# Kernel optimization log

Measured on AMD Instinct MI355X. Metric: run time of the kernel, lower is better.

Reference implementation:

```python
import jax, jax.numpy as jnp
import numpy as np
import math

S, B, H, NH = 2048, 2, 2048, 16
HD = H // NH
COEFF = 1.0  # layer_number = 1
NORM = math.sqrt(HD) * COEFF
MASK_VAL = -10000.0


def setup_inputs() -> dict:
    key = jax.random.key(0)
    ks = jax.random.split(key, 4)
    hidden_states = jax.random.normal(ks[0], (S, B, H), dtype=jnp.float32)
    # causal mask: True = masked (Megatron convention)
    attention_mask = jnp.triu(jnp.ones((S, S), dtype=bool), k=1)[None, None]
    w_qkv = jax.random.normal(ks[1], (H, 3 * H), dtype=jnp.float32) * (1.0 / math.sqrt(H))
    b_qkv = jnp.zeros((3 * H,), dtype=jnp.float32)
    w_dense = jax.random.normal(ks[2], (H, H), dtype=jnp.float32) * (1.0 / math.sqrt(H))
    b_dense = jnp.zeros((H,), dtype=jnp.float32)
    return {"hidden_states": hidden_states, "attention_mask": attention_mask,
            "w_qkv": w_qkv, "b_qkv": b_qkv, "w_dense": w_dense, "b_dense": b_dense}


def reference(hidden_states, attention_mask, w_qkv, b_qkv, w_dense, b_dense):
    s, b, h = hidden_states.shape
    # QKV projection: [s, b, 3h] -> [s, b, nh, 3*hd] -> split
    mixed = hidden_states @ w_qkv + b_qkv
    mixed = mixed.reshape(s, b, NH, 3 * HD)
    q, k, v = jnp.split(mixed, 3, axis=-1)  # each [s, b, nh, hd]
    # raw scores scaled by 1/(sqrt(hd)*coeff)  -> [b, nh, s_q, s_k]
    scores = jnp.einsum('sbnd,tbnd->bnst', q, k) / NORM
    # fused scale-mask-softmax in fp32 with scale=coeff (net 1/sqrt(hd))
    scores32 = scores.astype(jnp.float32) * COEFF
    scores32 = jnp.where(attention_mask, MASK_VAL, scores32)
    probs = jax.nn.softmax(scores32, axis=-1).astype(hidden_states.dtype)
    # dropout p=0.0 -> identity
    context = jnp.einsum('bnst,tbnd->sbnd', probs, v).reshape(s, b, h)
    # row-parallel dense with skip_bias_add: bias returned separately
    output = context @ w_dense
    return output, b_dense
```

## Files before the change

### kernel.cpp

```cpp
#include <hip/hip_runtime.h>
#include <hip/hip_bf16.h>

constexpr int S   = 2048;
constexpr int B   = 2;
constexpr int H   = 2048;
constexpr int NH  = 16;
constexpr int HD  = 128;
constexpr int K3H = 3 * H;
constexpr float SCALE2 = 0.08838834764831845f * 1.4426950408889634f;
constexpr float MSHIFT = 12.0f;

typedef __attribute__((ext_vector_type(8))) short short8;
typedef __attribute__((ext_vector_type(4))) float f32x4;

__device__ __forceinline__ ushort f2b(float f) {
  uint u = __float_as_uint(f);
  return (ushort)((u + 0x7fffu + ((u >> 16) & 1u)) >> 16);
}

__device__ __forceinline__ f32x4 mfma16(short8 a, short8 b, f32x4 c) {
  return __builtin_amdgcn_mfma_f32_16x16x32_bf16(a, b, c, 0, 0, 0);
}

__device__ __forceinline__ void gld16(const ushort* g, ushort* l) {
  __builtin_amdgcn_global_load_lds((const __attribute__((address_space(1))) void*)g,
                                   (__attribute__((address_space(3))) void*)l,
                                   16, 0, 0);
}

__global__ __launch_bounds__(256) void cast_bf16(const float* __restrict__ src,
                                                 ushort* __restrict__ dst, int n) {
  int i = (blockIdx.x * 256 + threadIdx.x) * 4;
  if (i >= n) return;
  float4 v = *(const float4*)(src + i);
  ushort4 o;
  o.x = f2b(v.x); o.y = f2b(v.y); o.z = f2b(v.z); o.w = f2b(v.w);
  *(ushort4*)(dst + i) = o;
}

__global__ __launch_bounds__(256) void transpose_cast(const float* __restrict__ src,
                                                      ushort* __restrict__ dst,
                                                      int R, int C) {
  __shared__ ushort tile[32][33];
  int c0 = blockIdx.x * 32, r0 = blockIdx.y * 32;
  int tx = threadIdx.x, ty = threadIdx.y;
#pragma unroll
  for (int i = 0; i < 4; i++) {
    int r = r0 + ty + i * 8;
    tile[ty + i * 8][tx] = f2b(src[(size_t)r * C + c0 + tx]);
  }
  __syncthreads();
#pragma unroll
  for (int i = 0; i < 4; i++) {
    int c = c0 + ty + i * 8;
    dst[(size_t)c * R + r0 + tx] = tile[tx][ty + i * 8];
  }
}

template <int MODE>
__global__ __launch_bounds__(256) void gemm_bt(const ushort* __restrict__ A,
                                               const ushort* __restrict__ Bt,
                                               const float* __restrict__ bias,
                                               void* __restrict__ out0,
                                               void* __restrict__ out1,
                                               int M, int N, int K) {
  __shared__ ushort lds_a[128 * 32];
  __shared__ ushort lds_b[128 * 32];
  const int tid  = threadIdx.x;
  const int wave = tid >> 6, lane = tid & 63;
  const int quad = lane >> 4, l15 = lane & 15;
  const int wr = wave >> 1, wc = wave & 1;
  const int m0 = blockIdx.y * 128, n0 = blockIdx.x * 128;

  f32x4 acc[4][4] = {};

  const int crow = lane >> 2;
  const int ccol = ((lane & 3) ^ ((crow >> 1) & 3)) * 8;
  const ushort* ga0 = A  + (size_t)(m0 + wave * 16 + crow) * K + ccol;
  const ushort* ga1 = A  + (size_t)(m0 + (wave + 4) * 16 + crow) * K + ccol;
  const ushort* gb0 = Bt + (size_t)(n0 + wave * 16 + crow) * K + ccol;
  const ushort* gb1 = Bt + (size_t)(n0 + (wave + 4) * 16 + crow) * K + ccol;
  ushort* la0 = &lds_a[wave * 512];
  ushort* la1 = &lds_a[(wave + 4) * 512];
  ushort* lb0 = &lds_b[wave * 512];
  ushort* lb1 = &lds_b[(wave + 4) * 512];

  const int swz = ((l15 >> 1) & 3);

  const int nk = K >> 5;
  for (int kt = 0; kt < nk; kt++) {
    const int ko = kt * 32;
    gld16(ga0 + ko, la0);
    gld16(ga1 + ko, la1);
    gld16(gb0 + ko, lb0);
    gld16(gb1 + ko, lb1);
    __syncthreads();

    short8 af[4], bq[4];
#pragma unroll
    for (int mt = 0; mt < 4; mt++)
      af[mt] = *(const short8*)&lds_a[(wr * 64 + mt * 16 + l15) * 32 + (quad ^ swz) * 8];
#pragma unroll
    for (int nt = 0; nt < 4; nt++)
      bq[nt] = *(const short8*)&lds_b[(wc * 64 + nt * 16 + l15) * 32 + (quad ^ swz) * 8];
#pragma unroll
    for (int mt = 0; mt < 4; mt++)
#pragma unroll
      for (int nt = 0; nt < 4; nt++)
        acc[mt][nt] = mfma16(af[mt], bq[nt], acc[mt][nt]);
    __syncthreads();
  }

  if (MODE == 1) {
#pragma unroll
    for (int nt = 0; nt < 4; nt++) {
      const int col = n0 + wc * 64 + nt * 16 + l15;
      const int nh  = col / 384;
      const int rem = col - nh * 384;
      const float bv = bias[col];
      if (rem < 256) {
        ushort* qk = (ushort*)out0;
#pragma unroll
        for (int mt = 0; mt < 4; mt++) {
          const int rb = m0 + wr * 64 + mt * 16 + quad * 4;
#pragma unroll
          for (int i = 0; i < 4; i++)
            qk[((size_t)(rb + i) * NH + nh) * 256 + rem] = f2b(acc[mt][nt][i] + bv);
        }
      } else {
        ushort* vt = (ushort*)out1;
        const size_t colbase = ((size_t)nh * 128 + (rem - 256)) * S;
#pragma unroll
        for (int mt = 0; mt < 4; mt++) {
          const int rb = m0 + wr * 64 + mt * 16 + quad * 4;
#pragma unroll
          for (int i = 0; i < 4; i++) {
            const int row = rb + i;
            vt[(size_t)(row & 1) * ((size_t)NH * 128 * S) + colbase + (row >> 1)]
                = f2b(acc[mt][nt][i] + bv);
          }
        }
      }
    }
  } else {
    float* Co = (float*)out0;
#pragma unroll
    for (int mt = 0; mt < 4; mt++)
#pragma unroll
      for (int nt = 0; nt < 4; nt++) {
        const int col = n0 + wc * 64 + nt * 16 + l15;
#pragma unroll
        for (int i = 0; i < 4; i++) {
          const int row = m0 + wr * 64 + mt * 16 + quad * 4 + i;
          Co[(size_t)row * N + col] = acc[mt][nt][i];
        }
      }
  }
}

__global__ __launch_bounds__(256) void flash_attn(const ushort* __restrict__ qkb,
                                                  const ushort* __restrict__ VtG,
                                                  ushort* __restrict__ ctxb) {
  __shared__ ushort Ks[2][64 * 128];
  __shared__ ushort Vt[2][128 * 64];
  __shared__ ushort Pls[4][16 * 64];

  const int tid  = threadIdx.x;
  const int wave = tid >> 6, lane = tid & 63;
  const int quad = lane >> 4, l15 = lane & 15;
  const int jj = blockIdx.x;
  const int nh = blockIdx.y, b = blockIdx.z;
  const int qtA = jj, qtB = 31 - jj;
  const int p0len = jj + 1;
  constexpr int TOT = 33;

  ushort* Pw = Pls[wave];

  const ushort* kSrc[4];
  const ushort* vSrc[4];
#pragma unroll
  for (int j = 0; j < 4; j++) {
    const int tK = wave * 16 + j * 4 + quad;
    const int cK = l15 ^ (j * 4 + quad);
    kSrc[j] = qkb + (((size_t)(tK * B + b) * NH + nh) * 256 + 128 + cK * 8);
    const int dV = wave * 32 + j * 8 + (lane >> 3);
    const int c2 = (lane & 7) ^ ((lane >> 3) & 7);
    vSrc[j] = VtG + ((size_t)(b * NH + nh) * 128 + dV) * (size_t)S + c2 * 8;
  }
  const size_t kStep = (size_t)64 * B * NH * 256;

  auto tile_kt = [&](int it) { return it < p0len ? it : it - p0len; };

  auto stageTile = [&](int kt, int nxt) {
    const size_t ko = (size_t)kt * kStep;
    const int vo = kt * 64;
#pragma unroll
    for (int j = 0; j < 4; j++)
      gld16(kSrc[j] + ko, &Ks[nxt][(wave * 256 + j * 64) * 8]);
#pragma unroll
    for (int j = 0; j < 4; j++)
      gld16(vSrc[j] + vo, &Vt[nxt][(wave * 256 + j * 64) * 8]);
  };

  short8 qf[4];
  int q0 = qtA * 64;
  {
    const ushort* qPtr = qkb + (((size_t)((q0 + wave * 16 + l15) * B + b) * NH + nh) * 256 + quad * 8);
#pragma unroll
    for (int ks = 0; ks < 4; ks++) qf[ks] = *(const short8*)(qPtr + ks * 32);
  }

  float l_r[4];
  f32x4 acc_o[8];
#pragma unroll
  for (int i = 0; i < 4; i++) l_r[i] = 0.0f;
#pragma unroll
  for (int j = 0; j < 8; j++) acc_o[j] = (f32x4){0.f, 0.f, 0.f, 0.f};

  stageTile(0, 0);
  __syncthreads();

  for (int it = 0; it < TOT; it++) {
    const int buf = it & 1;
    const int t0 = tile_kt(it) * 64;

    if (it + 1 < TOT) stageTile(tile_kt(it + 1), buf ^ 1);

    f32x4 sa[4];
#pragma unroll
    for (int nt = 0; nt < 4; nt++) sa[nt] = (f32x4){0.f, 0.f, 0.f, 0.f};
#pragma unroll
    for (int ks = 0; ks < 4; ks++) {
#pragma unroll
      for (int nt = 0; nt < 4; nt++) {
        const int gs = (ks * 4 + quad) ^ l15;
        short8 bq = *(const short8*)&Ks[buf][((nt * 16 + l15) * 16 + gs) * 8];
        sa[nt] = mfma16(qf[ks], bq, sa[nt]);
      }
    }

    const bool diag = (it == jj) || (it == TOT - 1);
#pragma unroll
    for (int i = 0; i < 4; i++) {
      const int qg = q0 + wave * 16 + quad * 4 + i;
      const int prow = quad * 4 + i;
      float lacc = l_r[i];
#pragma unroll
      for (int nt = 0; nt < 4; nt++) {
        float e = fmaf(sa[nt][i], SCALE2, -MSHIFT);
        if (diag) {
          const int tg = t0 + nt * 16 + l15;
          if (tg > qg) e = -1e30f;
        }
        const float p = exp2f(e);
        lacc += p;
        const int gs = (nt * 2 + (l15 >> 3)) ^ (prow & 7);
        Pw[prow * 64 + gs * 8 + (l15 & 7)] = f2b(p);
      }
      l_r[i] = lacc;
    }

#pragma unroll
    for (int ks2 = 0; ks2 < 2; ks2++) {
      const int pg = (ks2 * 4 + quad) ^ (l15 & 7);
      short8 a2 = *(const short8*)&Pw[l15 * 64 + pg * 8];
#pragma unroll
      for (int j = 0; j < 8; j++) {
        const int gs = (ks2 * 4 + quad) ^ (l15 & 7);
        short8 b2 = *(const short8*)&Vt[buf][((j * 16 + l15) * 8 + gs) * 8];
        acc_o[j] = mfma16(a2, b2, acc_o[j]);
      }
    }

    if (it == jj) {
#pragma unroll
      for (int i = 0; i < 4; i++) {
        float ls = l_r[i];
#pragma unroll
        for (int off = 1; off < 16; off <<= 1) ls += __shfl_xor(ls, off);
        const float inv = 1.0f / ls;
        const int qg = q0 + wave * 16 + quad * 4 + i;
        ushort* dst = ctxb + ((size_t)qg * B + b) * H + nh * HD;
#pragma unroll
        for (int j = 0; j < 8; j++)
          dst[j * 16 + l15] = f2b(acc_o[j][i] * inv);
      }
      q0 = qtB * 64;
      const ushort* qPtr = qkb + (((size_t)((q0 + wave * 16 + l15) * B + b) * NH + nh) * 256 + quad * 8);
#pragma unroll
      for (int ks = 0; ks < 4; ks++) qf[ks] = *(const short8*)(qPtr + ks * 32);
#pragma unroll
      for (int i = 0; i < 4; i++) l_r[i] = 0.0f;
#pragma unroll
      for (int j = 0; j < 8; j++) acc_o[j] = (f32x4){0.f, 0.f, 0.f, 0.f};
    }

    __syncthreads();
  }

#pragma unroll
  for (int i = 0; i < 4; i++) {
    float ls = l_r[i];
#pragma unroll
    for (int off = 1; off < 16; off <<= 1) ls += __shfl_xor(ls, off);
    const float inv = 1.0f / ls;
    const int qg = q0 + wave * 16 + quad * 4 + i;
    ushort* dst = ctxb + ((size_t)qg * B + b) * H + nh * HD;
#pragma unroll
    for (int j = 0; j < 8; j++)
      dst[j * 16 + l15] = f2b(acc_o[j][i] * inv);
  }
}

extern "C" void kernel_launch(void* const* d_in, const int* in_sizes, int n_in,
                              void* d_out, int out_size, void* d_ws, size_t ws_size,
                              hipStream_t stream) {
  (void)in_sizes; (void)n_in; (void)out_size; (void)ws_size;
  const float* hs     = (const float*)d_in[0];
  const float* wqkv   = (const float*)d_in[2];
  const float* bqkv   = (const float*)d_in[3];
  const float* wdense = (const float*)d_in[4];
  const float* bdense = (const float*)d_in[5];
  float* out = (float*)d_out;

  ushort* Xb      = (ushort*)d_ws;
  ushort* WqkvT   = Xb      + (size_t)S * B * H;
  ushort* WdenseT = WqkvT   + (size_t)H * K3H;
  ushort* qkb     = WdenseT + (size_t)H * H;
  ushort* VtG     = qkb     + (size_t)S * B * NH * 256;
  ushort* ctxb    = VtG     + (size_t)B * NH * HD * S;

  cast_bf16<<<dim3((S * B * H) / 1024), dim3(256), 0, stream>>>(hs, Xb, S * B * H);
  transpose_cast<<<dim3(K3H / 32, H / 32), dim3(32, 8), 0, stream>>>(wqkv, WqkvT, H, K3H);
  transpose_cast<<<dim3(H / 32, H / 32), dim3(32, 8), 0, stream>>>(wdense, WdenseT, H, H);

  gemm_bt<1><<<dim3(K3H / 128, (S * B) / 128), dim3(256), 0, stream>>>(
      Xb, WqkvT, bqkv, qkb, VtG, S * B, K3H, H);

  flash_attn<<<dim3(16, NH, B), dim3(256), 0, stream>>>(qkb, VtG, ctxb);

  gemm_bt<0><<<dim3(H / 128, (S * B) / 128), dim3(256), 0, stream>>>(
      ctxb, WdenseT, nullptr, out, nullptr, S * B, H, H);

  hipMemcpyAsync(out + (size_t)S * B * H, bdense, H * sizeof(float),
                 hipMemcpyDeviceToDevice, stream);
}
```

Measured before the change: 438.6 us.

## Deepen GEMM K-tile to 64 and use 128-row query tiles in attention

The GEMM now stages a 64-wide K slice per iteration with a row-based XOR swizzle. This halves the number of barrier-separated loop iterations and doubles LDS usage per block. The flash attention kernel moves to 512 threads (8 waves), so each block handles 128-query tiles in pairs, and each staged K/V tile is shared by twice as many query rows. In exchange the grid has half as many blocks, the causal mask check runs per wave, and a wave whose query rows end before the key tile still does the masked work for it.

```diff
diff --git a/kernel.cpp b/kernel.cpp
--- a/kernel.cpp
+++ b/kernel.cpp
@@ -64,8 +64,8 @@
                                                void* __restrict__ out0,
                                                void* __restrict__ out1,
                                                int M, int N, int K) {
-  __shared__ ushort lds_a[128 * 32];
-  __shared__ ushort lds_b[128 * 32];
+  __shared__ ushort lds_a[128 * 64];
+  __shared__ ushort lds_b[128 * 64];
   const int tid  = threadIdx.x;
   const int wave = tid >> 6, lane = tid & 63;
   const int quad = lane >> 4, l15 = lane & 15;
@@ -74,40 +74,38 @@
 
   f32x4 acc[4][4] = {};
 
-  const int crow = lane >> 2;
-  const int ccol = ((lane & 3) ^ ((crow >> 1) & 3)) * 8;
-  const ushort* ga0 = A  + (size_t)(m0 + wave * 16 + crow) * K + ccol;
-  const ushort* ga1 = A  + (size_t)(m0 + (wave + 4) * 16 + crow) * K + ccol;
-  const ushort* gb0 = Bt + (size_t)(n0 + wave * 16 + crow) * K + ccol;
-  const ushort* gb1 = Bt + (size_t)(n0 + (wave + 4) * 16 + crow) * K + ccol;
-  ushort* la0 = &lds_a[wave * 512];
-  ushort* la1 = &lds_a[(wave + 4) * 512];
-  ushort* lb0 = &lds_b[wave * 512];
-  ushort* lb1 = &lds_b[(wave + 4) * 512];
-
-  const int swz = ((l15 >> 1) & 3);
-
-  const int nk = K >> 5;
+  const int srow   = tid >> 3;
+  const int schunk = (tid & 7) ^ (srow & 7);
+  const ushort* gaS = A  + (size_t)(m0 + srow) * K + schunk * 8;
+  const ushort* gbS = Bt + (size_t)(n0 + srow) * K + schunk * 8;
+
+  const int fsw = l15 & 7;
+
+  const int nk = K >> 6;
   for (int kt = 0; kt < nk; kt++) {
-    const int ko = kt * 32;
-    gld16(ga0 + ko, la0);
-    gld16(ga1 + ko, la1);
-    gld16(gb0 + ko, lb0);
-    gld16(gb1 + ko, lb1);
+    const int ko = kt * 64;
+#pragma unroll
+    for (int j = 0; j < 4; j++) {
+      gld16(gaS + (size_t)(j * 32) * K + ko, &lds_a[(j * 256 + wave * 64) * 8]);
+      gld16(gbS + (size_t)(j * 32) * K + ko, &lds_b[(j * 256 + wave * 64) * 8]);
+    }
     __syncthreads();
 
-    short8 af[4], bq[4];
-#pragma unroll
-    for (int mt = 0; mt < 4; mt++)
-      af[mt] = *(const short8*)&lds_a[(wr * 64 + mt * 16 + l15) * 32 + (quad ^ swz) * 8];
-#pragma unroll
-    for (int nt = 0; nt < 4; nt++)
-      bq[nt] = *(const short8*)&lds_b[(wc * 64 + nt * 16 + l15) * 32 + (quad ^ swz) * 8];
-#pragma unroll
-    for (int mt = 0; mt < 4; mt++)
+#pragma unroll
+    for (int ks = 0; ks < 2; ks++) {
+      short8 af[4], bq[4];
+#pragma unroll
+      for (int mt = 0; mt < 4; mt++)
+        af[mt] = *(const short8*)&lds_a[((wr * 64 + mt * 16 + l15) * 8 + ((ks * 4 + quad) ^ fsw)) * 8];
 #pragma unroll
       for (int nt = 0; nt < 4; nt++)
-        acc[mt][nt] = mfma16(af[mt], bq[nt], acc[mt][nt]);
+        bq[nt] = *(const short8*)&lds_b[((wc * 64 + nt * 16 + l15) * 8 + ((ks * 4 + quad) ^ fsw)) * 8];
+#pragma unroll
+      for (int mt = 0; mt < 4; mt++)
+#pragma unroll
+        for (int nt = 0; nt < 4; nt++)
+          acc[mt][nt] = mfma16(af[mt], bq[nt], acc[mt][nt]);
+    }
     __syncthreads();
   }
 
@@ -158,52 +156,46 @@
   }
 }
 
-__global__ __launch_bounds__(256) void flash_attn(const ushort* __restrict__ qkb,
+__global__ __launch_bounds__(512) void flash_attn(const ushort* __restrict__ qkb,
                                                   const ushort* __restrict__ VtG,
                                                   ushort* __restrict__ ctxb) {
   __shared__ ushort Ks[2][64 * 128];
   __shared__ ushort Vt[2][128 * 64];
-  __shared__ ushort Pls[4][16 * 64];
+  __shared__ ushort Pls[8][16 * 64];
 
   const int tid  = threadIdx.x;
   const int wave = tid >> 6, lane = tid & 63;
   const int quad = lane >> 4, l15 = lane & 15;
   const int jj = blockIdx.x;
   const int nh = blockIdx.y, b = blockIdx.z;
-  const int qtA = jj, qtB = 31 - jj;
-  const int p0len = jj + 1;
-  constexpr int TOT = 33;
+  const int stA = jj, stB = 15 - jj;
+  const int nA = 2 * jj + 2;
+  constexpr int TOT = 34;
 
   ushort* Pw = Pls[wave];
 
-  const ushort* kSrc[4];
-  const ushort* vSrc[4];
-#pragma unroll
-  for (int j = 0; j < 4; j++) {
-    const int tK = wave * 16 + j * 4 + quad;
-    const int cK = l15 ^ (j * 4 + quad);
-    kSrc[j] = qkb + (((size_t)(tK * B + b) * NH + nh) * 256 + 128 + cK * 8);
-    const int dV = wave * 32 + j * 8 + (lane >> 3);
-    const int c2 = (lane & 7) ^ ((lane >> 3) & 7);
-    vSrc[j] = VtG + ((size_t)(b * NH + nh) * 128 + dV) * (size_t)S + c2 * 8;
-  }
-  const size_t kStep = (size_t)64 * B * NH * 256;
-
-  auto tile_kt = [&](int it) { return it < p0len ? it : it - p0len; };
+  const int ktRow = tid >> 4;
+  const int kCol  = (tid & 15) ^ (ktRow & 15);
+  const ushort* kS = qkb + (((size_t)(ktRow * B + b) * NH + nh) * 256 + 128 + kCol * 8);
+  const int vdRow = tid >> 3;
+  const int vCol  = (tid & 7) ^ (vdRow & 7);
+  const ushort* vS = VtG + ((size_t)(b * NH + nh) * 128 + vdRow) * (size_t)S + vCol * 8;
+
+  const size_t kRowStep32 = (size_t)32 * B * NH * 256;
+  const size_t vRowStep64 = (size_t)64 * S;
+  const size_t kTileStep  = (size_t)64 * B * NH * 256;
 
   auto stageTile = [&](int kt, int nxt) {
-    const size_t ko = (size_t)kt * kStep;
+    const size_t ko = (size_t)kt * kTileStep;
     const int vo = kt * 64;
-#pragma unroll
-    for (int j = 0; j < 4; j++)
-      gld16(kSrc[j] + ko, &Ks[nxt][(wave * 256 + j * 64) * 8]);
-#pragma unroll
-    for (int j = 0; j < 4; j++)
-      gld16(vSrc[j] + vo, &Vt[nxt][(wave * 256 + j * 64) * 8]);
+    gld16(kS + ko, &Ks[nxt][(wave * 64) * 8]);
+    gld16(kS + ko + kRowStep32, &Ks[nxt][(512 + wave * 64) * 8]);
+    gld16(vS + vo, &Vt[nxt][(wave * 64) * 8]);
+    gld16(vS + vo + vRowStep64, &Vt[nxt][(512 + wave * 64) * 8]);
   };
 
   short8 qf[4];
-  int q0 = qtA * 64;
+  int q0 = stA * 128;
   {
     const ushort* qPtr = qkb + (((size_t)((q0 + wave * 16 + l15) * B + b) * NH + nh) * 256 + quad * 8);
 #pragma unroll
@@ -222,9 +214,11 @@
 
   for (int it = 0; it < TOT; it++) {
     const int buf = it & 1;
-    const int t0 = tile_kt(it) * 64;
-
-    if (it + 1 < TOT) stageTile(tile_kt(it + 1), buf ^ 1);
+    const int kt = (it < nA) ? it : it - nA;
+    const int t0 = kt * 64;
+
+    if (it + 1 < TOT)
+      stageTile((it + 1 < nA) ? it + 1 : it + 1 - nA, buf ^ 1);
 
     f32x4 sa[4];
 #pragma unroll
@@ -239,10 +233,11 @@
       }
     }
 
-    const bool diag = (it == jj) || (it == TOT - 1);
+    const int qw0 = q0 + wave * 16;
+    const bool diag = (t0 + 63 > qw0);
 #pragma unroll
     for (int i = 0; i < 4; i++) {
-      const int qg = q0 + wave * 16 + quad * 4 + i;
+      const int qg = qw0 + quad * 4 + i;
       const int prow = quad * 4 + i;
       float lacc = l_r[i];
 #pragma unroll
@@ -272,7 +267,7 @@
       }
     }
 
-    if (it == jj) {
+    if (it == nA - 1) {
 #pragma unroll
       for (int i = 0; i < 4; i++) {
         float ls = l_r[i];
@@ -285,7 +280,7 @@
         for (int j = 0; j < 8; j++)
           dst[j * 16 + l15] = f2b(acc_o[j][i] * inv);
       }
-      q0 = qtB * 64;
+      q0 = stB * 128;
       const ushort* qPtr = qkb + (((size_t)((q0 + wave * 16 + l15) * B + b) * NH + nh) * 256 + quad * 8);
 #pragma unroll
       for (int ks = 0; ks < 4; ks++) qf[ks] = *(const short8*)(qPtr + ks * 32);
@@ -337,7 +332,7 @@
   gemm_bt<1><<<dim3(K3H / 128, (S * B) / 128), dim3(256), 0, stream>>>(
       Xb, WqkvT, bqkv, qkb, VtG, S * B, K3H, H);
 
-  flash_attn<<<dim3(16, NH, B), dim3(256), 0, stream>>>(qkb, VtG, ctxb);
+  flash_attn<<<dim3(8, NH, B), dim3(512), 0, stream>>>(qkb, VtG, ctxb);
 
   gemm_bt<0><<<dim3(H / 128, (S * B) / 128), dim3(256), 0, stream>>>(
       ctxb, WdenseT, nullptr, out, nullptr, S * B, H, H);
```

Result: faster. 404.0 us (-7.9%).
